# Optimization experiments

Hardware: AMD Instinct MI355X
Metric: run time of the kernel (lower is better)

The kernel has to match this reference:

```python
import jax, jax.numpy as jnp
import numpy as np

B, T, D = 16, 4096, 1024
HID = 4 * D // 3  # 1365, per SelectorMLP(hidden=4*d//3)
RHO, TAU, LN_EPS = 0.2, 1.0, 1e-5


def setup_inputs() -> dict:
    key = jax.random.key(0)
    ks = jax.random.split(key, 6)
    embeddings = jax.random.normal(ks[0], (B, T, D), dtype=jnp.float32)
    attn = (jax.random.uniform(ks[1], (B, T)) < 0.9).astype(jnp.float32)
    ln_w = jnp.ones((D,), jnp.float32)
    ln_b = jnp.zeros((D,), jnp.float32)
    fc1_w = jax.random.normal(ks[2], (HID, D), jnp.float32) * (1.0 / np.sqrt(D))
    fc1_b = jnp.zeros((HID,), jnp.float32)
    fc2_w = jax.random.normal(ks[3], (1, HID), jnp.float32) * (1.0 / np.sqrt(HID))
    fc2_b = jnp.zeros((1,), jnp.float32)
    return {"embeddings": embeddings, "attn": attn, "ln_w": ln_w, "ln_b": ln_b,
            "fc1_w": fc1_w, "fc1_b": fc1_b, "fc2_w": fc2_w, "fc2_b": fc2_b}


def _hard_topk(z, K):
    # z: [B,T], K: [B,1] float integer budgets -> exact top-K 0/1 mask per row
    b, t = z.shape
    order = jnp.argsort(-z, axis=1)                       # descending sort indices
    mask = (jnp.arange(t)[None, :] < K).astype(z.dtype)   # [B,T] first-K ranks
    h = jnp.zeros_like(z).at[jnp.arange(b)[:, None], order].set(mask)
    return h


def reference(embeddings, attn, ln_w, ln_b, fc1_w, fc1_b, fc2_w, fc2_b):
    emb = embeddings * attn[:, :, None]                    # [B,T,D]
    # SelectorMLP (dropout = identity in eval)
    mu = jnp.mean(emb, axis=-1, keepdims=True)
    var = jnp.mean(jnp.square(emb - mu), axis=-1, keepdims=True)
    x = (emb - mu) / jnp.sqrt(var + LN_EPS) * ln_w + ln_b
    x = jax.nn.gelu(jnp.einsum('btd,hd->bth', x, fc1_w) + fc1_b, approximate=False)
    scores = jnp.einsum('bth,oh->bto', x, fc2_w)[..., 0] + fc2_b[0]  # [B,T]
    scores = jnp.where(attn == 0, -1e9, scores)
    p = jax.nn.softmax(scores / TAU, axis=1)
    entropy = -jnp.sum(p * jnp.log(p + 1e-12), axis=1)     # [B]
    T_eff = jnp.clip(jnp.sum(attn, axis=1), 1, None)
    norm_entropy = jnp.mean(entropy / jnp.log(T_eff))
    T_eff2 = jnp.sum(attn, axis=1, keepdims=True)          # [B,1]
    K = jnp.clip(jnp.round(RHO * T_eff2), 1, None)
    z = K * p
    h = _hard_topk(z, K)
    g = h + (z - jax.lax.stop_gradient(z))                 # straight-through
    return g, z, norm_entropy
```

## Files before the change

kernel.cpp:

```cpp
#include <hip/hip_runtime.h>
#include <math.h>

#define B_ 16
#define T_ 4096
#define D_ 1024
#define HID_ 1365
#define NPAD 1408
#define NGRP 88
#define N_TOK (B_*T_)
#define RHO_ 0.2f
#define LN_EPS_ 1e-5f
#define SC 1024.0f
#define INV_SC2 (1.0f/(1024.0f*1024.0f))

#define NHT 11
#define WCHUNKS (NGRP*32*4*16)
#define NG16 4096
#define ACHUNKS ((size_t)NG16*32*64)

typedef _Float16 f16x8 __attribute__((ext_vector_type(8)));
typedef _Float16 f16x4 __attribute__((ext_vector_type(4)));
typedef float f32x4 __attribute__((ext_vector_type(4)));

__global__ __launch_bounds__(256) void ln_stats_kernel(
    const float* __restrict__ emb, const float* __restrict__ attn,
    float* __restrict__ mu, float* __restrict__ rstd)
{
  int tid = threadIdx.x;
  int wave = tid >> 6, lane = tid & 63;
  int token = blockIdx.x * 4 + wave;
  const float* p = emb + (size_t)token * D_;
  float a = attn[token];
  float s = 0.f, sq = 0.f;
#pragma unroll
  for (int q = 0; q < 4; ++q) {
    float4 v = *reinterpret_cast<const float4*>(p + lane * 4 + q * 256);
    v.x *= a; v.y *= a; v.z *= a; v.w *= a;
    s  += v.x + v.y + v.z + v.w;
    sq += v.x * v.x + v.y * v.y + v.z * v.z + v.w * v.w;
  }
#pragma unroll
  for (int off = 32; off > 0; off >>= 1) {
    s  += __shfl_down(s, off, 64);
    sq += __shfl_down(sq, off, 64);
  }
  if (lane == 0) {
    float m = s * (1.f / D_);
    float var = sq * (1.f / D_) - m * m;
    if (var < 0.f) var = 0.f;
    mu[token] = m;
    rstd[token] = 1.f / sqrtf(var + LN_EPS_);
  }
}

__global__ __launch_bounds__(256) void wsplit_kernel(
    const float* __restrict__ fc1w, f16x8* __restrict__ whi, f16x8* __restrict__ wlo)
{
  int c = blockIdx.x * 256 + threadIdx.x;
  if (c >= WCHUNKS) return;
  int ln = c & 15, q = (c >> 4) & 3, ks = (c >> 6) & 31, g = c >> 11;
  int n = g * 16 + ln;
  int k = ks * 32 + q * 8;
  f16x8 hi, lo;
#pragma unroll
  for (int j = 0; j < 8; ++j) {
    float v = (n < HID_) ? fc1w[(size_t)n * D_ + k + j] * SC : 0.f;
    _Float16 h = (_Float16)v;
    hi[j] = h;
    lo[j] = (_Float16)(v - (float)h);
  }
  whi[c] = hi;
  wlo[c] = lo;
}

#define ASTRIDE 516
__global__ __launch_bounds__(256) void asplit_kernel(
    const float* __restrict__ emb, const float* __restrict__ attn,
    const float* __restrict__ mu, const float* __restrict__ rstd,
    const float* __restrict__ lnw, const float* __restrict__ lnb,
    f16x8* __restrict__ ahi, f16x8* __restrict__ alo)
{
  __shared__ float tile[16 * ASTRIDE];
  int tid = threadIdx.x;
  int g = blockIdx.x >> 1, kh = blockIdx.x & 1;
  int kbase = kh * 512;
#pragma unroll
  for (int it = 0; it < 8; ++it) {
    int idx = tid + it * 256;
    int row = idx >> 7, c4 = idx & 127;
    float4 v = *reinterpret_cast<const float4*>(
        emb + (size_t)(g * 16 + row) * D_ + kbase + c4 * 4);
    *reinterpret_cast<float4*>(&tile[row * ASTRIDE + c4 * 4]) = v;
  }
  __syncthreads();
#pragma unroll
  for (int it = 0; it < 4; ++it) {
    int idx = tid + it * 256;
    int ksl = idx >> 6, l = idx & 63;
    int ln = l & 15, q = l >> 4;
    int token = g * 16 + ln;
    float a = attn[token], rs = rstd[token];
    float alpha = a * rs;
    float nmr = -mu[token] * rs;
    int colbase = ksl * 32 + q * 8;
    float4 e0 = *reinterpret_cast<const float4*>(&tile[ln * ASTRIDE + colbase]);
    float4 e1 = *reinterpret_cast<const float4*>(&tile[ln * ASTRIDE + colbase + 4]);
    float ev[8] = {e0.x, e0.y, e0.z, e0.w, e1.x, e1.y, e1.z, e1.w};
    f16x8 hi, lo;
#pragma unroll
    for (int j = 0; j < 8; ++j) {
      int kg = kbase + colbase + j;
      float wv = lnw[kg], bv = lnb[kg];
      float y = fmaf(ev[j] * alpha, wv, fmaf(nmr, wv, bv)) * SC;
      _Float16 h = (_Float16)y;
      hi[j] = h;
      lo[j] = (_Float16)(y - (float)h);
    }
    size_t c = (size_t)(g * 32 + kh * 16 + ksl) * 64 + l;
    ahi[c] = hi;
    alo[c] = lo;
  }
}

__global__ __launch_bounds__(256, 2) void mfma_score_v4(
    const f16x8* __restrict__ ahi, const f16x8* __restrict__ alo,
    const f16x8* __restrict__ whi, const f16x8* __restrict__ wlo,
    const float* __restrict__ fc1b, const float* __restrict__ fc2w,
    float* __restrict__ partial)
{
  __shared__ float red[2][128];
  int tid = threadIdx.x, lane = tid & 63;
  int w = tid >> 6, wrow = w & 1, wcol = w >> 1;
  int flat = blockIdx.x;
  int xcd = flat & 7, j = flat >> 3;
  int tb = xcd * 64 + j / NHT;
  int ht = j % NHT;
  int g0 = tb * 8 + wrow * 4;
  int gb0 = ht * 8 + wcol * 4;
  int ln16 = lane & 15, quad = lane >> 4;

  f32x4 acc[4][4];
#pragma unroll
  for (int i = 0; i < 4; ++i)
#pragma unroll
    for (int j2 = 0; j2 < 4; ++j2) acc[i][j2] = (f32x4)0.f;

#pragma unroll 2
  for (int ks = 0; ks < 32; ++ks) {
    size_t bbase = (size_t)(gb0 * 32 + ks) * 64 + lane;
    f16x8 bh[4], bl[4];
#pragma unroll
    for (int nj = 0; nj < 4; ++nj) {
      bh[nj] = whi[bbase + nj * 2048];
      bl[nj] = wlo[bbase + nj * 2048];
    }
    size_t abase = (size_t)(g0 * 32 + ks) * 64 + lane;
    f16x8 ah[4], al[4];
#pragma unroll
    for (int mi = 0; mi < 4; ++mi) {
      ah[mi] = ahi[abase + mi * 2048];
      al[mi] = alo[abase + mi * 2048];
    }
#pragma unroll
    for (int mi = 0; mi < 4; ++mi)
#pragma unroll
      for (int nj = 0; nj < 4; ++nj) {
        acc[mi][nj] = __builtin_amdgcn_mfma_f32_16x16x32_f16(ah[mi], bh[nj], acc[mi][nj], 0, 0, 0);
        acc[mi][nj] = __builtin_amdgcn_mfma_f32_16x16x32_f16(al[mi], bh[nj], acc[mi][nj], 0, 0, 0);
        acc[mi][nj] = __builtin_amdgcn_mfma_f32_16x16x32_f16(ah[mi], bl[nj], acc[mi][nj], 0, 0, 0);
      }
  }

  float s[4][4];
#pragma unroll
  for (int mi = 0; mi < 4; ++mi)
#pragma unroll
    for (int r = 0; r < 4; ++r) s[mi][r] = 0.f;
#pragma unroll
  for (int nj = 0; nj < 4; ++nj) {
    int h = (gb0 + nj) * 16 + ln16;
    float b1 = 0.f, w2 = 0.f;
    if (h < HID_) { b1 = fc1b[h]; w2 = fc2w[h]; }
#pragma unroll
    for (int mi = 0; mi < 4; ++mi)
#pragma unroll
      for (int r = 0; r < 4; ++r) {
        float v = acc[mi][nj][r] * INV_SC2 + b1;
        float gel = 0.5f * v * (1.f + erff(v * 0.70710678118654752440f));
        s[mi][r] = fmaf(gel, w2, s[mi][r]);
      }
  }
#pragma unroll
  for (int mi = 0; mi < 4; ++mi)
#pragma unroll
    for (int r = 0; r < 4; ++r) {
      float v = s[mi][r];
      v += __shfl_xor(v, 1, 64);
      v += __shfl_xor(v, 2, 64);
      v += __shfl_xor(v, 4, 64);
      v += __shfl_xor(v, 8, 64);
      s[mi][r] = v;
    }
  if (ln16 == 0) {
#pragma unroll
    for (int mi = 0; mi < 4; ++mi)
#pragma unroll
      for (int r = 0; r < 4; ++r)
        red[wcol][wrow * 64 + mi * 16 + quad * 4 + r] = s[mi][r];
  }
  __syncthreads();
  if (tid < 128)
    partial[(size_t)ht * N_TOK + tb * 128 + tid] = red[0][tid] + red[1][tid];
}

__global__ __launch_bounds__(1024) void softmax_kernel(
    const float* __restrict__ partial, const float* __restrict__ fc2b,
    const float* __restrict__ attn,
    float* __restrict__ out_z, float* __restrict__ rowent, float* __restrict__ rowK)
{
  __shared__ float buf[1024];
  int b = blockIdx.x, tid = threadIdx.x;
  const float* arow = attn + b * T_;
  float sv[4], av[4];
  float f2b = fc2b[0];
#pragma unroll
  for (int q = 0; q < 4; ++q) {
    int t = tid + q * 1024;
    av[q] = arow[t];
    float sc = f2b;
#pragma unroll
    for (int p = 0; p < NHT; ++p) sc += partial[(size_t)p * N_TOK + b * T_ + t];
    sv[q] = (av[q] == 0.f) ? -1e9f : sc;
  }
  float m = fmaxf(fmaxf(sv[0], sv[1]), fmaxf(sv[2], sv[3]));
  buf[tid] = m; __syncthreads();
  for (int s = 512; s > 0; s >>= 1) { if (tid < s) buf[tid] = fmaxf(buf[tid], buf[tid + s]); __syncthreads(); }
  m = buf[0]; __syncthreads();
  float e[4]; float es = 0.f, as = 0.f;
#pragma unroll
  for (int q = 0; q < 4; ++q) { e[q] = expf(sv[q] - m); es += e[q]; as += av[q]; }
  buf[tid] = es; __syncthreads();
  for (int s = 512; s > 0; s >>= 1) { if (tid < s) buf[tid] += buf[tid + s]; __syncthreads(); }
  es = buf[0]; __syncthreads();
  buf[tid] = as; __syncthreads();
  for (int s = 512; s > 0; s >>= 1) { if (tid < s) buf[tid] += buf[tid + s]; __syncthreads(); }
  as = buf[0]; __syncthreads();
  float K = fmaxf(1.f, rintf(RHO_ * as));
  float inv = 1.f / es;
  float ent = 0.f;
#pragma unroll
  for (int q = 0; q < 4; ++q) {
    float p = e[q] * inv;
    out_z[b * T_ + tid + q * 1024] = K * p;
    ent -= p * logf(p + 1e-12f);
  }
  buf[tid] = ent; __syncthreads();
  for (int s = 512; s > 0; s >>= 1) { if (tid < s) buf[tid] += buf[tid + s]; __syncthreads(); }
  if (tid == 0) {
    rowent[b] = buf[0] / logf(fmaxf(as, 1.f));
    rowK[b] = K;
  }
}

__global__ __launch_bounds__(1024) void topk_kernel(
    const float* __restrict__ zall, float* __restrict__ g,
    const float* __restrict__ rowent, const float* __restrict__ rowK,
    float* __restrict__ out_scalar)
{
  __shared__ float sm[T_];
  __shared__ int s_first, s_last;
  int b = blockIdx.x, tid = threadIdx.x;
  const float* zrow = zall + b * T_;
  for (int t = tid; t < T_; t += 1024) sm[t] = zrow[t];
  __syncthreads();
  for (int k = 2; k <= T_; k <<= 1) {
    for (int j = k >> 1; j > 0; j >>= 1) {
      for (int t = tid; t < T_; t += 1024) {
        int ixj = t ^ j;
        if (ixj > t) {
          float a = sm[t], c = sm[ixj];
          bool desc = ((t & k) == 0);
          if (desc ? (a < c) : (a > c)) { sm[t] = c; sm[ixj] = a; }
        }
      }
      __syncthreads();
    }
  }
  int K = (int)rowK[b];
  float thr = sm[K - 1];
  if (tid == 0) { s_first = T_; s_last = -1; }
  __syncthreads();
  for (int t = tid; t < T_; t += 1024) {
    if (sm[t] == thr) { atomicMin(&s_first, t); atomicMax(&s_last, t); }
  }
  __syncthreads();
  int cgt = s_first;
  int eqTotal = s_last - s_first + 1;
  int need = K - cgt;
  float* grow = g + b * T_;
  bool allEq = (eqTotal == need);
  for (int t = tid; t < T_; t += 1024) {
    float zv = zrow[t];
    if (zv > thr) grow[t] = 1.f;
    else if (zv < thr) grow[t] = 0.f;
    else if (allEq) grow[t] = 1.f;
  }
  __syncthreads();
  if (!allEq && tid == 0) {
    int cnt = 0;
    for (int t = 0; t < T_; ++t) {
      float zv = zrow[t];
      if (zv == thr) { grow[t] = (cnt < need) ? 1.f : 0.f; ++cnt; }
    }
  }
  if (b == 0 && tid == 0) {
    float s = 0.f;
    for (int i = 0; i < B_; ++i) s += rowent[i];
    out_scalar[0] = s * (1.f / B_);
  }
}

extern "C" void kernel_launch(void* const* d_in, const int* in_sizes, int n_in,
                              void* d_out, int out_size, void* d_ws, size_t ws_size,
                              hipStream_t stream)
{
  const float* emb  = (const float*)d_in[0];
  const float* attn = (const float*)d_in[1];
  const float* lnw  = (const float*)d_in[2];
  const float* lnb  = (const float*)d_in[3];
  const float* fc1w = (const float*)d_in[4];
  const float* fc1b = (const float*)d_in[5];
  const float* fc2w = (const float*)d_in[6];
  const float* fc2b = (const float*)d_in[7];

  float* out = (float*)d_out;
  float* g  = out;
  float* z  = out + N_TOK;
  float* ns = out + 2 * N_TOK;

  float* mu      = (float*)d_ws;
  float* rstd    = mu + N_TOK;
  float* partial = rstd + N_TOK;
  float* rowent  = partial + (size_t)NHT * N_TOK;
  float* rowK    = rowent + 16;
  f16x8* whi     = (f16x8*)(rowK + 16);
  f16x8* wlo     = whi + WCHUNKS;
  f16x8* ahi     = wlo + WCHUNKS;
  f16x8* alo     = ahi + ACHUNKS;

  ln_stats_kernel<<<N_TOK / 4, 256, 0, stream>>>(emb, attn, mu, rstd);
  wsplit_kernel<<<(WCHUNKS + 255) / 256, 256, 0, stream>>>(fc1w, whi, wlo);
  asplit_kernel<<<NG16 * 2, 256, 0, stream>>>(emb, attn, mu, rstd, lnw, lnb, ahi, alo);
  mfma_score_v4<<<8 * 64 * NHT, 256, 0, stream>>>(ahi, alo, whi, wlo, fc1b, fc2w, partial);
  softmax_kernel<<<B_, 1024, 0, stream>>>(partial, fc2b, attn, z, rowent, rowK);
  topk_kernel<<<B_, 1024, 0, stream>>>(z, g, rowent, rowK, ns);
}
```

Before: 1.179 ms.

## Fuse LayerNorm stats into A-split and stage GEMM tiles via LDS double-buffering

Merges the LayerNorm statistics kernel into the A-operand split kernel, so each block loads a full 16-token row tile once into shared memory and computes mean and rstd there. This removes one full read of the embeddings and the mu/rstd round trip. The MFMA score kernel now stages A and B hi/lo fragments through double-buffered LDS using global_load_lds, with each wave loading one of the four operand arrays. Data shared between waves is then fetched once per block instead of by each wave from global memory, at the cost of a block barrier per k-step and 64KB of LDS, which may limit occupancy.

```diff
diff --git a/kernel.cpp b/kernel.cpp
--- a/kernel.cpp
+++ b/kernel.cpp
@@ -19,38 +19,12 @@
 #define ACHUNKS ((size_t)NG16*32*64)
 
 typedef _Float16 f16x8 __attribute__((ext_vector_type(8)));
-typedef _Float16 f16x4 __attribute__((ext_vector_type(4)));
 typedef float f32x4 __attribute__((ext_vector_type(4)));
 
-__global__ __launch_bounds__(256) void ln_stats_kernel(
-    const float* __restrict__ emb, const float* __restrict__ attn,
-    float* __restrict__ mu, float* __restrict__ rstd)
-{
-  int tid = threadIdx.x;
-  int wave = tid >> 6, lane = tid & 63;
-  int token = blockIdx.x * 4 + wave;
-  const float* p = emb + (size_t)token * D_;
-  float a = attn[token];
-  float s = 0.f, sq = 0.f;
-#pragma unroll
-  for (int q = 0; q < 4; ++q) {
-    float4 v = *reinterpret_cast<const float4*>(p + lane * 4 + q * 256);
-    v.x *= a; v.y *= a; v.z *= a; v.w *= a;
-    s  += v.x + v.y + v.z + v.w;
-    sq += v.x * v.x + v.y * v.y + v.z * v.z + v.w * v.w;
-  }
-#pragma unroll
-  for (int off = 32; off > 0; off >>= 1) {
-    s  += __shfl_down(s, off, 64);
-    sq += __shfl_down(sq, off, 64);
-  }
-  if (lane == 0) {
-    float m = s * (1.f / D_);
-    float var = sq * (1.f / D_) - m * m;
-    if (var < 0.f) var = 0.f;
-    mu[token] = m;
-    rstd[token] = 1.f / sqrtf(var + LN_EPS_);
-  }
+__device__ __forceinline__ void gl16(const void* g, void* l) {
+  __builtin_amdgcn_global_load_lds(
+      (const __attribute__((address_space(1))) unsigned int*)g,
+      (__attribute__((address_space(3))) unsigned int*)l, 16, 0, 0);
 }
 
 __global__ __launch_bounds__(256) void wsplit_kernel(
@@ -73,61 +47,86 @@
   wlo[c] = lo;
 }
 
-#define ASTRIDE 516
-__global__ __launch_bounds__(256) void asplit_kernel(
+#define FSTR 1028
+__global__ __launch_bounds__(256, 2) void lnasplit_kernel(
     const float* __restrict__ emb, const float* __restrict__ attn,
-    const float* __restrict__ mu, const float* __restrict__ rstd,
     const float* __restrict__ lnw, const float* __restrict__ lnb,
     f16x8* __restrict__ ahi, f16x8* __restrict__ alo)
 {
-  __shared__ float tile[16 * ASTRIDE];
+  __shared__ float tile[16 * FSTR];
+  __shared__ float smu[16], srs[16];
   int tid = threadIdx.x;
-  int g = blockIdx.x >> 1, kh = blockIdx.x & 1;
-  int kbase = kh * 512;
+  int g = blockIdx.x;
+  int wave = tid >> 6, lane = tid & 63;
+#pragma unroll
+  for (int it = 0; it < 16; ++it) {
+    int idx = tid + it * 256;
+    int row = idx >> 8, c4 = idx & 255;
+    float a = attn[g * 16 + row];
+    float4 v = *reinterpret_cast<const float4*>(
+        emb + (size_t)(g * 16 + row) * D_ + c4 * 4);
+    v.x *= a; v.y *= a; v.z *= a; v.w *= a;
+    *reinterpret_cast<float4*>(&tile[row * FSTR + c4 * 4]) = v;
+  }
+  __syncthreads();
+#pragma unroll
+  for (int r4 = 0; r4 < 4; ++r4) {
+    int row = wave * 4 + r4;
+    float s = 0.f, sq = 0.f;
+#pragma unroll
+    for (int q = 0; q < 4; ++q) {
+      float4 v = *reinterpret_cast<const float4*>(&tile[row * FSTR + lane * 4 + q * 256]);
+      s  += v.x + v.y + v.z + v.w;
+      sq += v.x * v.x + v.y * v.y + v.z * v.z + v.w * v.w;
+    }
+#pragma unroll
+    for (int off = 32; off > 0; off >>= 1) {
+      s  += __shfl_down(s, off, 64);
+      sq += __shfl_down(sq, off, 64);
+    }
+    if (lane == 0) {
+      float m = s * (1.f / D_);
+      float var = sq * (1.f / D_) - m * m;
+      if (var < 0.f) var = 0.f;
+      smu[row] = m;
+      srs[row] = 1.f / sqrtf(var + LN_EPS_);
+    }
+  }
+  __syncthreads();
 #pragma unroll
   for (int it = 0; it < 8; ++it) {
-    int idx = tid + it * 256;
-    int row = idx >> 7, c4 = idx & 127;
-    float4 v = *reinterpret_cast<const float4*>(
-        emb + (size_t)(g * 16 + row) * D_ + kbase + c4 * 4);
-    *reinterpret_cast<float4*>(&tile[row * ASTRIDE + c4 * 4]) = v;
-  }
-  __syncthreads();
-#pragma unroll
-  for (int it = 0; it < 4; ++it) {
     int idx = tid + it * 256;
     int ksl = idx >> 6, l = idx & 63;
     int ln = l & 15, q = l >> 4;
-    int token = g * 16 + ln;
-    float a = attn[token], rs = rstd[token];
-    float alpha = a * rs;
-    float nmr = -mu[token] * rs;
+    float rs = srs[ln];
+    float nmr = -smu[ln] * rs;
     int colbase = ksl * 32 + q * 8;
-    float4 e0 = *reinterpret_cast<const float4*>(&tile[ln * ASTRIDE + colbase]);
-    float4 e1 = *reinterpret_cast<const float4*>(&tile[ln * ASTRIDE + colbase + 4]);
+    float4 e0 = *reinterpret_cast<const float4*>(&tile[ln * FSTR + colbase]);
+    float4 e1 = *reinterpret_cast<const float4*>(&tile[ln * FSTR + colbase + 4]);
     float ev[8] = {e0.x, e0.y, e0.z, e0.w, e1.x, e1.y, e1.z, e1.w};
     f16x8 hi, lo;
 #pragma unroll
     for (int j = 0; j < 8; ++j) {
-      int kg = kbase + colbase + j;
+      int kg = colbase + j;
       float wv = lnw[kg], bv = lnb[kg];
-      float y = fmaf(ev[j] * alpha, wv, fmaf(nmr, wv, bv)) * SC;
+      float y = fmaf(ev[j] * rs, wv, fmaf(nmr, wv, bv)) * SC;
       _Float16 h = (_Float16)y;
       hi[j] = h;
       lo[j] = (_Float16)(y - (float)h);
     }
-    size_t c = (size_t)(g * 32 + kh * 16 + ksl) * 64 + l;
+    size_t c = (size_t)(g * 32 + ksl) * 64 + l;
     ahi[c] = hi;
     alo[c] = lo;
   }
 }
 
-__global__ __launch_bounds__(256, 2) void mfma_score_v4(
+__global__ __launch_bounds__(256, 2) void mfma_score_v5(
     const f16x8* __restrict__ ahi, const f16x8* __restrict__ alo,
     const f16x8* __restrict__ whi, const f16x8* __restrict__ wlo,
     const float* __restrict__ fc1b, const float* __restrict__ fc2w,
     float* __restrict__ partial)
 {
+  __shared__ f16x8 sbuf[2][2048];
   __shared__ float red[2][128];
   int tid = threadIdx.x, lane = tid & 63;
   int w = tid >> 6, wrow = w & 1, wcol = w >> 1;
@@ -135,31 +134,44 @@
   int xcd = flat & 7, j = flat >> 3;
   int tb = xcd * 64 + j / NHT;
   int ht = j % NHT;
-  int g0 = tb * 8 + wrow * 4;
-  int gb0 = ht * 8 + wcol * 4;
+  int g0 = tb * 8;
+  int hb0 = ht * 8;
   int ln16 = lane & 15, quad = lane >> 4;
 
+  const f16x8* src = (w == 0) ? ahi : (w == 1) ? alo : (w == 2) ? whi : wlo;
+  size_t grpbase = (w < 2) ? (size_t)g0 : (size_t)hb0;
+  const f16x8* sp = src + grpbase * 32 * 64 + lane;
+
+  auto STAGE = [&](int buf, int ks) {
+#pragma unroll
+    for (int i = 0; i < 8; ++i)
+      gl16(sp + (size_t)(i * 32 + ks) * 64, &sbuf[buf][w * 512 + i * 64]);
+  };
+
+  STAGE(0, 0);
+
   f32x4 acc[4][4];
 #pragma unroll
   for (int i = 0; i < 4; ++i)
 #pragma unroll
     for (int j2 = 0; j2 < 4; ++j2) acc[i][j2] = (f32x4)0.f;
+
+  __syncthreads();
 
 #pragma unroll 2
   for (int ks = 0; ks < 32; ++ks) {
-    size_t bbase = (size_t)(gb0 * 32 + ks) * 64 + lane;
-    f16x8 bh[4], bl[4];
+    int cur = ks & 1;
+    if (ks < 31) STAGE(cur ^ 1, ks + 1);
+    f16x8 ah[4], al[4], bh[4], bl[4];
+#pragma unroll
+    for (int mi = 0; mi < 4; ++mi) {
+      ah[mi] = sbuf[cur][(wrow * 4 + mi) * 64 + lane];
+      al[mi] = sbuf[cur][512 + (wrow * 4 + mi) * 64 + lane];
+    }
 #pragma unroll
     for (int nj = 0; nj < 4; ++nj) {
-      bh[nj] = whi[bbase + nj * 2048];
-      bl[nj] = wlo[bbase + nj * 2048];
-    }
-    size_t abase = (size_t)(g0 * 32 + ks) * 64 + lane;
-    f16x8 ah[4], al[4];
-#pragma unroll
-    for (int mi = 0; mi < 4; ++mi) {
-      ah[mi] = ahi[abase + mi * 2048];
-      al[mi] = alo[abase + mi * 2048];
+      bh[nj] = sbuf[cur][1024 + (wcol * 4 + nj) * 64 + lane];
+      bl[nj] = sbuf[cur][1536 + (wcol * 4 + nj) * 64 + lane];
     }
 #pragma unroll
     for (int mi = 0; mi < 4; ++mi)
@@ -169,8 +181,10 @@
         acc[mi][nj] = __builtin_amdgcn_mfma_f32_16x16x32_f16(al[mi], bh[nj], acc[mi][nj], 0, 0, 0);
         acc[mi][nj] = __builtin_amdgcn_mfma_f32_16x16x32_f16(ah[mi], bl[nj], acc[mi][nj], 0, 0, 0);
       }
-  }
-
+    __syncthreads();
+  }
+
+  int gb0 = hb0 + wcol * 4;
   float s[4][4];
 #pragma unroll
   for (int mi = 0; mi < 4; ++mi)
@@ -348,10 +362,9 @@
   f16x8* ahi     = wlo + WCHUNKS;
   f16x8* alo     = ahi + ACHUNKS;
 
-  ln_stats_kernel<<<N_TOK / 4, 256, 0, stream>>>(emb, attn, mu, rstd);
   wsplit_kernel<<<(WCHUNKS + 255) / 256, 256, 0, stream>>>(fc1w, whi, wlo);
-  asplit_kernel<<<NG16 * 2, 256, 0, stream>>>(emb, attn, mu, rstd, lnw, lnb, ahi, alo);
-  mfma_score_v4<<<8 * 64 * NHT, 256, 0, stream>>>(ahi, alo, whi, wlo, fc1b, fc2w, partial);
+  lnasplit_kernel<<<NG16, 256, 0, stream>>>(emb, attn, lnw, lnb, ahi, alo);
+  mfma_score_v5<<<8 * 64 * NHT, 256, 0, stream>>>(ahi, alo, whi, wlo, fc1b, fc2w, partial);
   softmax_kernel<<<B_, 1024, 0, stream>>>(partial, fc2b, attn, z, rowent, rowK);
   topk_kernel<<<B_, 1024, 0, stream>>>(z, g, rowent, rowK, ns);
 }
```

New measurement: 1.080 ms. 1.09x faster.
